# Kernel optimization log

Hardware: AMD Instinct MI355X
Metric: run time of the kernel (lower is better)

## Reference

```python
import jax, jax.numpy as jnp
import numpy as np

C = 0.01          # ToPoincare curvature hardcoded in get_dist
K = 5             # k_way (s0..s4 hardcoded in source)
N = 5             # n_shot
Q = 15            # queries per class -> LQ = K*Q = 75
D = 1024          # feature dim (hardcoded reshape(1,-1,1024))
TEMP = 1.0
N_AUG = 40
MIN_NORM = 1e-5


def _artanh(x):
    return jnp.arctanh(jnp.clip(x, -1 + 1e-5, 1 - 1e-5))


def _project(x, c):
    norm = jnp.maximum(jnp.linalg.norm(x, axis=-1, keepdims=True), MIN_NORM)
    maxnorm = (1 - 1e-3) / jnp.sqrt(c)
    return jnp.where(norm > maxnorm, x / norm * maxnorm, x)


def _expmap0(u, c):
    sc = jnp.sqrt(c)
    un = jnp.maximum(jnp.linalg.norm(u, axis=-1, keepdims=True), MIN_NORM)
    return jnp.tanh(sc * un) * u / (sc * un)


def _mobius_add(x, y, c):
    x2 = jnp.sum(x * x, -1, keepdims=True)
    y2 = jnp.sum(y * y, -1, keepdims=True)
    xy = jnp.sum(x * y, -1, keepdims=True)
    num = (1 + 2 * c * xy + c * y2) * x + (1 - c * x2) * y
    den = 1 + 2 * c * xy + c * c * x2 * y2
    return num / jnp.maximum(den, MIN_NORM)


def _expmap(x, u, c):
    # exp map at point x of tangent vector u
    sc = jnp.sqrt(c)
    un = jnp.maximum(jnp.linalg.norm(u, axis=-1, keepdims=True), MIN_NORM)
    lam = 2.0 / jnp.maximum(1 - c * jnp.sum(x * x, -1, keepdims=True), MIN_NORM)
    second = jnp.tanh(sc * lam * un / 2) * u / (sc * un)
    return _mobius_add(x, second, c)


def _ptransp0_p(x, v, c):
    # parallel transport of v from the origin to x
    return v * (1 - c * jnp.sum(x * x, -1, keepdims=True))


def _dist_matrix(x, y, c):
    # pairwise Poincare distance [n, m] without materializing [n,m,d]:
    # ||(-x) (+) y||^2 = a^2 x2 + b^2 y2 - 2ab<x,y>, a = 1-2c<x,y>+c y2, b = 1-c x2
    sc = jnp.sqrt(c)
    x2 = jnp.sum(x * x, -1)[:, None]
    y2 = jnp.sum(y * y, -1)[None, :]
    xy = x @ y.T
    a = 1 - 2 * c * xy + c * y2
    b = 1 - c * x2
    num2 = a * a * x2 + b * b * y2 - 2 * a * b * xy
    den = 1 - 2 * c * xy + c * c * x2 * y2
    norm = jnp.sqrt(jnp.maximum(num2, 0.0)) / jnp.maximum(den, MIN_NORM)
    return 2.0 / sc * _artanh(sc * norm)


def _p2k(x, c):
    return 2 * x / (1 + c * jnp.sum(x * x, -1, keepdims=True))


def _k2p(x, c):
    return x / (1 + jnp.sqrt(jnp.maximum(1 - c * jnp.sum(x * x, -1, keepdims=True), 0.0)))


def _poincare_mean_masked(x, mask, c):
    # Einstein-midpoint Poincare mean over rows of x weighted by {0,1} mask
    k = _p2k(x, c)
    lam = 1.0 / jnp.sqrt(jnp.maximum(1 - c * jnp.sum(k * k, -1), MIN_NORM))
    w = lam * mask
    mean_k = (w[:, None] * k).sum(0) / w.sum()
    return _k2p(mean_k, c)


def setup_inputs() -> dict:
    key = jax.random.key(0)
    k1, k2, k3 = jax.random.split(key, 3)
    feat = jax.random.normal(k1, (K * N + K * Q, D), dtype=jnp.float32)
    label = jax.random.randint(k2, (2, K * Q), 0, K)
    noise = jax.random.normal(k3, (K, N_AUG, D), dtype=jnp.float32)
    return {"feat": feat, "label": label, "noise": noise}


def reference(feat, label, noise):
    support_e = feat[: N * K].reshape(K, N, D)
    queries_e = feat[N * K:]                                  # [LQ, D]
    support_p_ = _project(_expmap0(feat[: N * K], C), C).reshape(K, N, D)
    queries_p = _project(_expmap0(queries_e, C), C)           # [LQ, D]

    ones_n = jnp.ones((N,), feat.dtype)
    proto_p = jax.vmap(lambda s: _poincare_mean_masked(s, ones_n, C))(support_p_)  # [K, D]
    dist = _dist_matrix(queries_p, proto_p, C) / TEMP          # [LQ, K]
    pred = jnp.argmax(-dist, 1)                                # [LQ]
    qmask = (pred[:, None] == jnp.arange(K)[None, :]).astype(feat.dtype)  # [LQ, K]

    def per_class(sup_p, sup_e, mq, nz):
        # sup_p/sup_e: [N,D]; mq: [LQ] routing mask; nz: [N_AUG,D] unit normals
        m = jnp.concatenate([ones_n, mq])                      # [N+LQ]
        pts_p = jnp.concatenate([sup_p, queries_p], 0)
        pts_e = jnp.concatenate([sup_e, queries_e], 0)
        s_p = _poincare_mean_masked(pts_p, m, C)               # [D] augmented proto
        cnt = m.sum()
        mu = (m[:, None] * pts_e).sum(0) / cnt
        var = (m[:, None] * (pts_e - mu) ** 2).sum(0) / (cnt - 1)  # unbiased, as torch.std
        std = jnp.sqrt(var)                                    # [D]
        v = nz * std                                           # torch.normal(0, std), 40 samples
        pt = _ptransp0_p(s_p[None, :], v, C)
        ex = _expmap(s_p[None, :], pt, C)                      # [N_AUG, D]
        s_new = jnp.concatenate([sup_p, ex], 0)                # [N+N_AUG, D]
        return _poincare_mean_masked(s_new, jnp.ones((N + N_AUG,), feat.dtype), C)

    proto_new = jax.vmap(per_class, in_axes=(0, 0, 1, 0))(support_p_, support_e, qmask, noise)
    dist_new = _dist_matrix(queries_p, proto_new, C) / TEMP

    y_pred = jax.nn.softmax(-dist_new, axis=1)
    log_p_y = jax.nn.log_softmax(-dist, axis=1)
    # nn.CrossEntropyLoss applied to log-probs (double log-softmax, faithful to source)
    ll = jax.nn.log_softmax(log_p_y, axis=1)
    lbl = label[1]
    loss = -jnp.mean(jnp.take_along_axis(ll, lbl[:, None], axis=1))
    return y_pred, loss
```

## Files before the change

### kernel.cpp

```cpp
#include <hip/hip_runtime.h>
#include <hip/hip_bf16.h>
#include <math.h>

#define CCd     0.01
#define SCd     0.1
#define MAXNRMd 9.99
#define MINNd   1e-5
#define DD      1024
#define NK      25
#define NQ      75
#define NROWS   100
#define KCLS    5
#define NAUG    40

__device__ __forceinline__ double wave_reduce_d(double v){
#pragma unroll
  for (int o = 32; o > 0; o >>= 1) v += __shfl_xor(v, o);
  return v;
}

__device__ __forceinline__ double hyp_dist_d(double xy, double x2, double y2){
  double a    = 1.0 - 2.0*CCd*xy + CCd*y2;
  double b    = 1.0 - CCd*x2;
  double num2 = a*a*x2 + b*b*y2 - 2.0*a*b*xy;
  double den  = 1.0 - 2.0*CCd*xy + CCd*CCd*x2*y2;
  double nrm  = sqrt(fmax(num2, 0.0)) / fmax(den, MINNd);
  double z    = SCd * nrm;
  z = fmin(fmax(z, -1.0 + MINNd), 1.0 - MINNd);
  return 10.0 * log((1.0 + z) / (1.0 - z));
}

__global__ __launch_bounds__(256)
void k_expmap(const float* __restrict__ feat, float* __restrict__ P,
              double* __restrict__ p2d){
  const int r = blockIdx.x, t = threadIdx.x;
  const float4 v = reinterpret_cast<const float4*>(feat + r*DD)[t];
  double ss = (double)v.x*v.x + (double)v.y*v.y + (double)v.z*v.z + (double)v.w*v.w;
  __shared__ double red[4];
  ss = wave_reduce_d(ss);
  if ((t & 63) == 0) red[t >> 6] = ss;
  __syncthreads();
  ss = red[0] + red[1] + red[2] + red[3];
  double un = fmax(sqrt(ss), MINNd);
  double th = tanh(SCd*un);
  double na = th * 10.0;
  double factor, pn;
  if (na > MAXNRMd) { factor = MAXNRMd/un; pn = MAXNRMd; }
  else              { factor = th/(SCd*un); pn = na; }
  float4 o;
  o.x = (float)(v.x*factor); o.y = (float)(v.y*factor);
  o.z = (float)(v.z*factor); o.w = (float)(v.w*factor);
  reinterpret_cast<float4*>(P + r*DD)[t] = o;
  if (t == 0) p2d[r] = pn*pn;
}

__global__ __launch_bounds__(1024)
void k_proto(const float* __restrict__ P, const double* __restrict__ p2d,
             float* __restrict__ protoP, double* __restrict__ proto2d){
  const int c = blockIdx.x, t = threadIdx.x;
  double la[5], wsum = 0.0;
#pragma unroll
  for (int i = 0; i < 5; i++){
    double pp = p2d[c*5+i];
    double a  = 2.0/(1.0 + CCd*pp);
    double k2 = a*a*pp;
    double l  = 1.0/sqrt(fmax(1.0 - CCd*k2, MINNd));
    la[i] = l*a; wsum += l;
  }
  double s = 0.0;
#pragma unroll
  for (int i = 0; i < 5; i++) s += la[i]*(double)P[(c*5+i)*DD + t];
  s /= wsum;
  __shared__ double red[16];
  double ss = wave_reduce_d(s*s);
  if ((t & 63) == 0) red[t >> 6] = ss;
  __syncthreads();
  ss = 0.0;
#pragma unroll
  for (int i = 0; i < 16; i++) ss += red[i];
  double sf = 1.0/(1.0 + sqrt(fmax(1.0 - CCd*ss, 0.0)));
  protoP[c*DD + t] = (float)(s*sf);
  if (t == 0) proto2d[c] = ss*sf*sf;
}

__global__ __launch_bounds__(256)
void k_dist1(const float* __restrict__ P, const float* __restrict__ protoP,
             const double* __restrict__ p2d, const double* __restrict__ proto2d,
             double* __restrict__ distS, int* __restrict__ predS){
  const int q = blockIdx.x, t = threadIdx.x;
  const float* xq = P + (NK+q)*DD;
  double acc[5] = {0,0,0,0,0};
#pragma unroll
  for (int k = 0; k < 4; k++){
    int d = t + 256*k;
    double x = (double)xq[d];
#pragma unroll
    for (int c = 0; c < 5; c++) acc[c] += x*(double)protoP[c*DD + d];
  }
  __shared__ double red[4][5];
#pragma unroll
  for (int c = 0; c < 5; c++) acc[c] = wave_reduce_d(acc[c]);
  if ((t & 63) == 0){
#pragma unroll
    for (int c = 0; c < 5; c++) red[t >> 6][c] = acc[c];
  }
  __syncthreads();
  if (t == 0){
    double x2 = p2d[NK+q];
    double best = 1e300; int bi = 0;
#pragma unroll
    for (int c = 0; c < 5; c++){
      double dot = red[0][c] + red[1][c] + red[2][c] + red[3][c];
      double dv  = hyp_dist_d(dot, x2, proto2d[c]);
      distS[q*5 + c] = dv;
      if (dv < best){ best = dv; bi = c; }
    }
    predS[q] = bi;
  }
}

__global__ __launch_bounds__(1024)
void k_aug(const float* __restrict__ feat, const float* __restrict__ noise,
           const float* __restrict__ P, const double* __restrict__ p2d,
           const int* __restrict__ predS,
           float* __restrict__ protoN, double* __restrict__ protoN2d){
  const int c = blockIdx.x, t = threadIdx.x;
  const int wave = t >> 6, lane = t & 63;
  __shared__ double wA[80], wL[80], wM[80];
  __shared__ int    rows[80];
  __shared__ double scal[8];
  __shared__ double spS[DD], stdS[DD];
  __shared__ double coefSj[NAUG], coefVj[NAUG], lamJ[NAUG];
  __shared__ double red[16];

  if (t < 80){
    int row; double m;
    if (t < 5){ row = c*5 + t; m = 1.0; }
    else      { row = NK + (t-5); m = (predS[t-5] == c) ? 1.0 : 0.0; }
    rows[t] = row;
    double pp = p2d[row];
    double a  = 2.0/(1.0 + CCd*pp);
    double k2 = a*a*pp;
    double l  = 1.0/sqrt(fmax(1.0 - CCd*k2, MINNd));
    wA[t] = m*l*a; wL[t] = m*l; wM[t] = m;
  }
  __syncthreads();
  if (t == 0){
    double wsum = 0.0, cnt = 0.0;
    for (int i = 0; i < 80; i++){ wsum += wL[i]; cnt += wM[i]; }
    scal[0] = wsum; scal[1] = cnt;
  }
  __syncthreads();
  const double wsum = scal[0], cnt = scal[1];

  {
    const int d = t;
    double mkd = 0.0, mud = 0.0, sqd = 0.0;
    for (int i = 0; i < 80; i++){
      int row = rows[i];
      mkd += wA[i]*(double)P[row*DD + d];
      double e = (double)feat[row*DD + d];
      mud += wM[i]*e;
      sqd += wM[i]*e*e;
    }
    mkd /= wsum;
    mud /= cnt;
    double var = (sqd - cnt*mud*mud)/(cnt - 1.0);
    stdS[d] = sqrt(fmax(var, 0.0));
    double s = wave_reduce_d(mkd*mkd);
    if (lane == 0) red[wave] = s;
    __syncthreads();
    double mk2 = 0.0;
#pragma unroll
    for (int i = 0; i < 16; i++) mk2 += red[i];
    double sf = 1.0/(1.0 + sqrt(fmax(1.0 - CCd*mk2, 0.0)));
    spS[d] = mkd*sf;
    if (t == 0) scal[2] = mk2*sf*sf;
  }
  __syncthreads();
  const double sp2  = scal[2];
  const double lamx = 2.0/fmax(1.0 - CCd*sp2, MINNd);
  const double ptf  = 1.0 - CCd*sp2;

  for (int j = wave; j < NAUG; j += 16){
    const float* nzr = noise + (c*NAUG + j)*DD;
    double s_un2 = 0.0, s_dot = 0.0;
#pragma unroll
    for (int k = 0; k < 16; k++){
      int d = lane + 64*k;
      double v = (double)nzr[d]*stdS[d];
      s_un2 += v*v;
      s_dot += v*spS[d];
    }
#pragma unroll
    for (int o = 32; o > 0; o >>= 1){
      s_un2 += __shfl_xor(s_un2, o);
      s_dot += __shfl_xor(s_dot, o);
    }
    if (lane == 0){
      double unv = sqrt(s_un2);
      double unp = fmax(ptf*unv, MINNd);
      double g0  = tanh(SCd*lamx*unp*0.5)/(SCd*unp);
      double g   = g0*ptf;
      double y2  = g*g*s_un2;
      double xy  = g*s_dot;
      double A   = 1.0 + 2.0*CCd*xy + CCd*y2;
      double B   = ptf;
      double den = fmax(1.0 + 2.0*CCd*xy + CCd*CCd*sp2*y2, MINNd);
      double ex2 = (A*A*sp2 + 2.0*A*B*g*s_dot + B*B*g*g*s_un2)/(den*den);
      double ae  = 2.0/(1.0 + CCd*ex2);
      double k2e = ae*ae*ex2;
      double le  = 1.0/sqrt(fmax(1.0 - CCd*k2e, MINNd));
      coefSj[j] = le*ae*A/den;
      coefVj[j] = le*ae*B*g/den;
      lamJ[j]   = le;
    }
  }
  __syncthreads();
  if (t == 0){
    double lsum = 0.0, sS = 0.0;
#pragma unroll
    for (int i = 0; i < 5; i++){
      double pp = p2d[c*5+i];
      double a  = 2.0/(1.0 + CCd*pp);
      double k2 = a*a*pp;
      double l  = 1.0/sqrt(fmax(1.0 - CCd*k2, MINNd));
      lsum += l;
    }
    for (int j = 0; j < NAUG; j++){ lsum += lamJ[j]; sS += coefSj[j]; }
    scal[3] = lsum; scal[4] = sS;
  }
  __syncthreads();
  const double lamsum = scal[3], sumS = scal[4];

  {
    const int d = t;
    double val = sumS*spS[d];
#pragma unroll
    for (int i = 0; i < 5; i++) val += wA[i]*(double)P[(c*5+i)*DD + d];
    double nacc = 0.0;
    for (int j = 0; j < NAUG; j++) nacc += coefVj[j]*(double)noise[(c*NAUG + j)*DD + d];
    val += stdS[d]*nacc;
    val /= lamsum;
    double s = wave_reduce_d(val*val);
    if (lane == 0) red[wave] = s;
    __syncthreads();
    double mk2 = 0.0;
#pragma unroll
    for (int i = 0; i < 16; i++) mk2 += red[i];
    double sf = 1.0/(1.0 + sqrt(fmax(1.0 - CCd*mk2, 0.0)));
    protoN[c*DD + d] = (float)(val*sf);
    if (t == 0) protoN2d[c] = mk2*sf*sf;
  }
}

__global__ __launch_bounds__(256)
void k_dist2(const float* __restrict__ P, const float* __restrict__ protoN,
             const double* __restrict__ p2d, const double* __restrict__ protoN2d,
             const double* __restrict__ distS, const int* __restrict__ label,
             float* __restrict__ out, double* __restrict__ lossQ){
  const int q = blockIdx.x, t = threadIdx.x;
  const float* xq = P + (NK+q)*DD;
  double acc[5] = {0,0,0,0,0};
#pragma unroll
  for (int k = 0; k < 4; k++){
    int d = t + 256*k;
    double x = (double)xq[d];
#pragma unroll
    for (int c = 0; c < 5; c++) acc[c] += x*(double)protoN[c*DD + d];
  }
  __shared__ double red[4][5];
#pragma unroll
  for (int c = 0; c < 5; c++) acc[c] = wave_reduce_d(acc[c]);
  if ((t & 63) == 0){
#pragma unroll
    for (int c = 0; c < 5; c++) red[t >> 6][c] = acc[c];
  }
  __syncthreads();
  if (t == 0){
    double x2 = p2d[NK+q];
    double v[5]; double mx = -1e300;
#pragma unroll
    for (int c = 0; c < 5; c++){
      double dot = red[0][c] + red[1][c] + red[2][c] + red[3][c];
      v[c] = -hyp_dist_d(dot, x2, protoN2d[c]);
      mx = fmax(mx, v[c]);
    }
    double se = 0.0;
#pragma unroll
    for (int c = 0; c < 5; c++){ v[c] = exp(v[c]-mx); se += v[c]; }
    double inv = 1.0/se;
#pragma unroll
    for (int c = 0; c < 5; c++) out[q*5 + c] = (float)(v[c]*inv);

    double u[5]; mx = -1e300;
#pragma unroll
    for (int c = 0; c < 5; c++){ u[c] = -distS[q*5+c]; mx = fmax(mx, u[c]); }
    double s1 = 0.0;
#pragma unroll
    for (int c = 0; c < 5; c++) s1 += exp(u[c]-mx);
    double lse1 = mx + log(s1);
#pragma unroll
    for (int c = 0; c < 5; c++) u[c] -= lse1;
    double mx2 = -1e300;
#pragma unroll
    for (int c = 0; c < 5; c++) mx2 = fmax(mx2, u[c]);
    double s2 = 0.0;
#pragma unroll
    for (int c = 0; c < 5; c++) s2 += exp(u[c]-mx2);
    double lse2 = mx2 + log(s2);
    lossQ[q] = u[label[NQ + q]] - lse2;
  }
}

__global__ __launch_bounds__(128)
void k_loss(const double* __restrict__ lossQ, float* __restrict__ out){
  const int t = threadIdx.x;
  double v = (t < NQ) ? lossQ[t] : 0.0;
  v = wave_reduce_d(v);
  __shared__ double red[2];
  if ((t & 63) == 0) red[t >> 6] = v;
  __syncthreads();
  if (t == 0) out[NQ*KCLS] = (float)(-(red[0]+red[1])/75.0);
}

extern "C" void kernel_launch(void* const* d_in, const int* in_sizes, int n_in,
                              void* d_out, int out_size, void* d_ws, size_t ws_size,
                              hipStream_t stream) {
  const float* feat  = (const float*)d_in[0];
  const int*   label = (const int*)d_in[1];
  const float* noise = (const float*)d_in[2];
  float* out = (float*)d_out;

  float*  P        = (float*)d_ws;
  float*  protoP   = P + NROWS*DD;
  float*  protoN   = protoP + KCLS*DD;
  double* p2d      = (double*)(protoN + KCLS*DD);
  double* proto2d  = p2d + NROWS;
  double* protoN2d = proto2d + KCLS;
  double* distS    = protoN2d + KCLS;
  double* lossQ    = distS + NQ*KCLS;
  int*    predS    = (int*)(lossQ + NQ);

  k_expmap<<<NROWS, 256, 0, stream>>>(feat, P, p2d);
  k_proto <<<KCLS, 1024, 0, stream>>>(P, p2d, protoP, proto2d);
  k_dist1 <<<NQ, 256, 0, stream>>>(P, protoP, p2d, proto2d, distS, predS);
  k_aug   <<<KCLS, 1024, 0, stream>>>(feat, noise, P, p2d, predS, protoN, protoN2d);
  k_dist2 <<<NQ, 256, 0, stream>>>(P, protoN, p2d, protoN2d, distS, label, out, lossQ);
  k_loss  <<<1, 128, 0, stream>>>(lossQ, out);
}
```

Measured before the change: 119.9 us.

## Split per-class augmentation kernel into stats, coef, assembly kernels across more blocks

The single 5-block k_aug kernel (1024 threads each) is replaced by three kernels: k_stats (20 blocks over feature chunks), k_coef (200 blocks, one per augmented sample) and k_asm (20 blocks). Normalisation scales are deferred, so partial squared norms are passed between kernels and the Klein-to-Poincare factor is applied later, including inside k_dist2. This spreads a serial, low-occupancy stage across many more CUs. It costs two extra launches and global round-trips for the intermediate std and mean vectors.

New measurement: 98.29 us. 18.0% less time.

```diff
diff --git a/kernel.cpp b/kernel.cpp
--- a/kernel.cpp
+++ b/kernel.cpp
@@ -28,6 +28,13 @@
   double z    = SCd * nrm;
   z = fmin(fmax(z, -1.0 + MINNd), 1.0 - MINNd);
   return 10.0 * log((1.0 + z) / (1.0 - z));
+}
+
+__device__ __forceinline__ void kweights(double pp, double* la, double* l_out){
+  double a  = 2.0/(1.0 + CCd*pp);
+  double k2 = a*a*pp;
+  double l  = 1.0/sqrt(fmax(1.0 - CCd*k2, MINNd));
+  *la = l*a; *l_out = l;
 }
 
 __global__ __launch_bounds__(256)
@@ -61,11 +68,9 @@
   double la[5], wsum = 0.0;
 #pragma unroll
   for (int i = 0; i < 5; i++){
-    double pp = p2d[c*5+i];
-    double a  = 2.0/(1.0 + CCd*pp);
-    double k2 = a*a*pp;
-    double l  = 1.0/sqrt(fmax(1.0 - CCd*k2, MINNd));
-    la[i] = l*a; wsum += l;
+    double lam;
+    kweights(p2d[c*5+i], &la[i], &lam);
+    wsum += lam;
   }
   double s = 0.0;
 #pragma unroll
@@ -119,30 +124,21 @@
   }
 }
 
-__global__ __launch_bounds__(1024)
-void k_aug(const float* __restrict__ feat, const float* __restrict__ noise,
-           const float* __restrict__ P, const double* __restrict__ p2d,
-           const int* __restrict__ predS,
-           float* __restrict__ protoN, double* __restrict__ protoN2d){
-  const int c = blockIdx.x, t = threadIdx.x;
-  const int wave = t >> 6, lane = t & 63;
-  __shared__ double wA[80], wL[80], wM[80];
-  __shared__ int    rows[80];
-  __shared__ double scal[8];
-  __shared__ double spS[DD], stdS[DD];
-  __shared__ double coefSj[NAUG], coefVj[NAUG], lamJ[NAUG];
-  __shared__ double red[16];
-
+__global__ __launch_bounds__(256)
+void k_stats(const float* __restrict__ feat, const float* __restrict__ P,
+             const double* __restrict__ p2d, const int* __restrict__ predS,
+             double* __restrict__ std_g, double* __restrict__ mkr_g,
+             double* __restrict__ mk2part){
+  const int c = blockIdx.x >> 2, chunk = blockIdx.x & 3, t = threadIdx.x;
+  __shared__ double wA[80], wL[80], wM[80], scal[2], red[4];
+  __shared__ int rows[80];
   if (t < 80){
     int row; double m;
     if (t < 5){ row = c*5 + t; m = 1.0; }
     else      { row = NK + (t-5); m = (predS[t-5] == c) ? 1.0 : 0.0; }
     rows[t] = row;
-    double pp = p2d[row];
-    double a  = 2.0/(1.0 + CCd*pp);
-    double k2 = a*a*pp;
-    double l  = 1.0/sqrt(fmax(1.0 - CCd*k2, MINNd));
-    wA[t] = m*l*a; wL[t] = m*l; wM[t] = m;
+    double la, l; kweights(p2d[row], &la, &l);
+    wA[t] = m*la; wL[t] = m*l; wM[t] = m;
   }
   __syncthreads();
   if (t == 0){
@@ -152,111 +148,117 @@
   }
   __syncthreads();
   const double wsum = scal[0], cnt = scal[1];
-
-  {
-    const int d = t;
-    double mkd = 0.0, mud = 0.0, sqd = 0.0;
-    for (int i = 0; i < 80; i++){
-      int row = rows[i];
-      mkd += wA[i]*(double)P[row*DD + d];
-      double e = (double)feat[row*DD + d];
-      mud += wM[i]*e;
-      sqd += wM[i]*e*e;
+  const int d = chunk*256 + t;
+  double mkd = 0.0, mud = 0.0, sqd = 0.0;
+  for (int i = 0; i < 80; i++){
+    int row = rows[i];
+    mkd += wA[i]*(double)P[row*DD + d];
+    double e = (double)feat[row*DD + d];
+    mud += wM[i]*e;
+    sqd += wM[i]*e*e;
+  }
+  mkd /= wsum;
+  mud /= cnt;
+  double var = (sqd - cnt*mud*mud)/(cnt - 1.0);
+  std_g[c*DD + d] = sqrt(fmax(var, 0.0));
+  mkr_g[c*DD + d] = mkd;
+  double s = wave_reduce_d(mkd*mkd);
+  if ((t & 63) == 0) red[t >> 6] = s;
+  __syncthreads();
+  if (t == 0) mk2part[blockIdx.x] = red[0] + red[1] + red[2] + red[3];
+}
+
+__global__ __launch_bounds__(256)
+void k_coef(const float* __restrict__ noise, const double* __restrict__ std_g,
+            const double* __restrict__ mkr_g, const double* __restrict__ mk2part,
+            double* __restrict__ coefS_g, double* __restrict__ coefV_g,
+            double* __restrict__ lamJ_g){
+  const int j = blockIdx.x, c = blockIdx.y, t = threadIdx.x;
+  const float*  nzr = noise + (c*NAUG + j)*DD;
+  const double* st  = std_g + c*DD;
+  const double* mk  = mkr_g + c*DD;
+  double un2 = 0.0, rd = 0.0;
+#pragma unroll
+  for (int k = 0; k < 4; k++){
+    int d = t + 256*k;
+    double v = (double)nzr[d]*st[d];
+    un2 += v*v;
+    rd  += v*mk[d];
+  }
+  __shared__ double red[4][2];
+  un2 = wave_reduce_d(un2);
+  rd  = wave_reduce_d(rd);
+  if ((t & 63) == 0){ red[t >> 6][0] = un2; red[t >> 6][1] = rd; }
+  __syncthreads();
+  if (t == 0){
+    double s_un2 = red[0][0]+red[1][0]+red[2][0]+red[3][0];
+    double rdot  = red[0][1]+red[1][1]+red[2][1]+red[3][1];
+    double mk2 = mk2part[c*4+0]+mk2part[c*4+1]+mk2part[c*4+2]+mk2part[c*4+3];
+    double sf  = 1.0/(1.0 + sqrt(fmax(1.0 - CCd*mk2, 0.0)));
+    double sp2 = mk2*sf*sf;
+    double lamx = 2.0/fmax(1.0 - CCd*sp2, MINNd);
+    double ptf  = 1.0 - CCd*sp2;
+    double s_dot = sf*rdot;
+    double unv = sqrt(s_un2);
+    double unp = fmax(ptf*unv, MINNd);
+    double g0  = tanh(SCd*lamx*unp*0.5)/(SCd*unp);
+    double g   = g0*ptf;
+    double y2  = g*g*s_un2;
+    double xy  = g*s_dot;
+    double A   = 1.0 + 2.0*CCd*xy + CCd*y2;
+    double B   = ptf;
+    double den = fmax(1.0 + 2.0*CCd*xy + CCd*CCd*sp2*y2, MINNd);
+    double ex2 = (A*A*sp2 + 2.0*A*B*g*s_dot + B*B*g*g*s_un2)/(den*den);
+    double ae  = 2.0/(1.0 + CCd*ex2);
+    double k2e = ae*ae*ex2;
+    double le  = 1.0/sqrt(fmax(1.0 - CCd*k2e, MINNd));
+    coefS_g[c*NAUG + j] = le*ae*A/den;
+    coefV_g[c*NAUG + j] = le*ae*B*g/den;
+    lamJ_g[c*NAUG + j]  = le;
+  }
+}
+
+__global__ __launch_bounds__(256)
+void k_asm(const float* __restrict__ noise, const float* __restrict__ P,
+           const double* __restrict__ p2d, const double* __restrict__ std_g,
+           const double* __restrict__ mkr_g, const double* __restrict__ mk2part,
+           const double* __restrict__ coefS_g, const double* __restrict__ coefV_g,
+           const double* __restrict__ lamJ_g,
+           float* __restrict__ protoNr, double* __restrict__ mk2Np){
+  const int c = blockIdx.x >> 2, chunk = blockIdx.x & 3, t = threadIdx.x;
+  __shared__ double cV[NAUG], supC[5], scal[3], red[4];
+  if (t < NAUG) cV[t] = coefV_g[c*NAUG + t];
+  if (t == 0){
+    double lsum = 0.0, sS = 0.0;
+#pragma unroll
+    for (int i = 0; i < 5; i++){
+      double la, l; kweights(p2d[c*5+i], &la, &l);
+      supC[i] = la; lsum += l;
     }
-    mkd /= wsum;
-    mud /= cnt;
-    double var = (sqd - cnt*mud*mud)/(cnt - 1.0);
-    stdS[d] = sqrt(fmax(var, 0.0));
-    double s = wave_reduce_d(mkd*mkd);
-    if (lane == 0) red[wave] = s;
-    __syncthreads();
-    double mk2 = 0.0;
-#pragma unroll
-    for (int i = 0; i < 16; i++) mk2 += red[i];
-    double sf = 1.0/(1.0 + sqrt(fmax(1.0 - CCd*mk2, 0.0)));
-    spS[d] = mkd*sf;
-    if (t == 0) scal[2] = mk2*sf*sf;
-  }
-  __syncthreads();
-  const double sp2  = scal[2];
-  const double lamx = 2.0/fmax(1.0 - CCd*sp2, MINNd);
-  const double ptf  = 1.0 - CCd*sp2;
-
-  for (int j = wave; j < NAUG; j += 16){
-    const float* nzr = noise + (c*NAUG + j)*DD;
-    double s_un2 = 0.0, s_dot = 0.0;
-#pragma unroll
-    for (int k = 0; k < 16; k++){
-      int d = lane + 64*k;
-      double v = (double)nzr[d]*stdS[d];
-      s_un2 += v*v;
-      s_dot += v*spS[d];
-    }
-#pragma unroll
-    for (int o = 32; o > 0; o >>= 1){
-      s_un2 += __shfl_xor(s_un2, o);
-      s_dot += __shfl_xor(s_dot, o);
-    }
-    if (lane == 0){
-      double unv = sqrt(s_un2);
-      double unp = fmax(ptf*unv, MINNd);
-      double g0  = tanh(SCd*lamx*unp*0.5)/(SCd*unp);
-      double g   = g0*ptf;
-      double y2  = g*g*s_un2;
-      double xy  = g*s_dot;
-      double A   = 1.0 + 2.0*CCd*xy + CCd*y2;
-      double B   = ptf;
-      double den = fmax(1.0 + 2.0*CCd*xy + CCd*CCd*sp2*y2, MINNd);
-      double ex2 = (A*A*sp2 + 2.0*A*B*g*s_dot + B*B*g*g*s_un2)/(den*den);
-      double ae  = 2.0/(1.0 + CCd*ex2);
-      double k2e = ae*ae*ex2;
-      double le  = 1.0/sqrt(fmax(1.0 - CCd*k2e, MINNd));
-      coefSj[j] = le*ae*A/den;
-      coefVj[j] = le*ae*B*g/den;
-      lamJ[j]   = le;
-    }
-  }
-  __syncthreads();
-  if (t == 0){
-    double lsum = 0.0, sS = 0.0;
-#pragma unroll
-    for (int i = 0; i < 5; i++){
-      double pp = p2d[c*5+i];
-      double a  = 2.0/(1.0 + CCd*pp);
-      double k2 = a*a*pp;
-      double l  = 1.0/sqrt(fmax(1.0 - CCd*k2, MINNd));
-      lsum += l;
-    }
-    for (int j = 0; j < NAUG; j++){ lsum += lamJ[j]; sS += coefSj[j]; }
-    scal[3] = lsum; scal[4] = sS;
-  }
-  __syncthreads();
-  const double lamsum = scal[3], sumS = scal[4];
-
-  {
-    const int d = t;
-    double val = sumS*spS[d];
-#pragma unroll
-    for (int i = 0; i < 5; i++) val += wA[i]*(double)P[(c*5+i)*DD + d];
-    double nacc = 0.0;
-    for (int j = 0; j < NAUG; j++) nacc += coefVj[j]*(double)noise[(c*NAUG + j)*DD + d];
-    val += stdS[d]*nacc;
-    val /= lamsum;
-    double s = wave_reduce_d(val*val);
-    if (lane == 0) red[wave] = s;
-    __syncthreads();
-    double mk2 = 0.0;
-#pragma unroll
-    for (int i = 0; i < 16; i++) mk2 += red[i];
-    double sf = 1.0/(1.0 + sqrt(fmax(1.0 - CCd*mk2, 0.0)));
-    protoN[c*DD + d] = (float)(val*sf);
-    if (t == 0) protoN2d[c] = mk2*sf*sf;
-  }
-}
-
-__global__ __launch_bounds__(256)
-void k_dist2(const float* __restrict__ P, const float* __restrict__ protoN,
-             const double* __restrict__ p2d, const double* __restrict__ protoN2d,
+    for (int j = 0; j < NAUG; j++){ lsum += lamJ_g[c*NAUG+j]; sS += coefS_g[c*NAUG+j]; }
+    double mk2 = mk2part[c*4+0]+mk2part[c*4+1]+mk2part[c*4+2]+mk2part[c*4+3];
+    double sf  = 1.0/(1.0 + sqrt(fmax(1.0 - CCd*mk2, 0.0)));
+    scal[0] = lsum; scal[1] = sS; scal[2] = sf;
+  }
+  __syncthreads();
+  const int d = chunk*256 + t;
+  double val = scal[1]*scal[2]*mkr_g[c*DD + d];
+#pragma unroll
+  for (int i = 0; i < 5; i++) val += supC[i]*(double)P[(c*5+i)*DD + d];
+  double na = 0.0;
+  for (int j = 0; j < NAUG; j++) na += cV[j]*(double)noise[(c*NAUG + j)*DD + d];
+  val += std_g[c*DD + d]*na;
+  val /= scal[0];
+  protoNr[c*DD + d] = (float)val;
+  double s = wave_reduce_d(val*val);
+  if ((t & 63) == 0) red[t >> 6] = s;
+  __syncthreads();
+  if (t == 0) mk2Np[blockIdx.x] = red[0] + red[1] + red[2] + red[3];
+}
+
+__global__ __launch_bounds__(256)
+void k_dist2(const float* __restrict__ P, const float* __restrict__ protoNr,
+             const double* __restrict__ p2d, const double* __restrict__ mk2Np,
              const double* __restrict__ distS, const int* __restrict__ label,
              float* __restrict__ out, double* __restrict__ lossQ){
   const int q = blockIdx.x, t = threadIdx.x;
@@ -267,7 +269,7 @@
     int d = t + 256*k;
     double x = (double)xq[d];
 #pragma unroll
-    for (int c = 0; c < 5; c++) acc[c] += x*(double)protoN[c*DD + d];
+    for (int c = 0; c < 5; c++) acc[c] += x*(double)protoNr[c*DD + d];
   }
   __shared__ double red[4][5];
 #pragma unroll
@@ -282,8 +284,11 @@
     double v[5]; double mx = -1e300;
 #pragma unroll
     for (int c = 0; c < 5; c++){
-      double dot = red[0][c] + red[1][c] + red[2][c] + red[3][c];
-      v[c] = -hyp_dist_d(dot, x2, protoN2d[c]);
+      double mk2N = mk2Np[c*4+0]+mk2Np[c*4+1]+mk2Np[c*4+2]+mk2Np[c*4+3];
+      double sfN  = 1.0/(1.0 + sqrt(fmax(1.0 - CCd*mk2N, 0.0)));
+      double dot  = sfN*(red[0][c] + red[1][c] + red[2][c] + red[3][c]);
+      double y2   = mk2N*sfN*sfN;
+      v[c] = -hyp_dist_d(dot, x2, y2);
       mx = fmax(mx, v[c]);
     }
     double se = 0.0;
@@ -334,18 +339,28 @@
 
   float*  P        = (float*)d_ws;
   float*  protoP   = P + NROWS*DD;
-  float*  protoN   = protoP + KCLS*DD;
-  double* p2d      = (double*)(protoN + KCLS*DD);
+  float*  protoNr  = protoP + KCLS*DD;
+  double* p2d      = (double*)(protoNr + KCLS*DD);
   double* proto2d  = p2d + NROWS;
-  double* protoN2d = proto2d + KCLS;
-  double* distS    = protoN2d + KCLS;
+  double* distS    = proto2d + KCLS;
   double* lossQ    = distS + NQ*KCLS;
-  int*    predS    = (int*)(lossQ + NQ);
+  double* std_g    = lossQ + NQ;
+  double* mkr_g    = std_g + KCLS*DD;
+  double* mk2part  = mkr_g + KCLS*DD;
+  double* coefS_g  = mk2part + 4*KCLS;
+  double* coefV_g  = coefS_g + KCLS*NAUG;
+  double* lamJ_g   = coefV_g + KCLS*NAUG;
+  double* mk2Np    = lamJ_g + KCLS*NAUG;
+  int*    predS    = (int*)(mk2Np + 4*KCLS);
 
   k_expmap<<<NROWS, 256, 0, stream>>>(feat, P, p2d);
   k_proto <<<KCLS, 1024, 0, stream>>>(P, p2d, protoP, proto2d);
   k_dist1 <<<NQ, 256, 0, stream>>>(P, protoP, p2d, proto2d, distS, predS);
-  k_aug   <<<KCLS, 1024, 0, stream>>>(feat, noise, P, p2d, predS, protoN, protoN2d);
-  k_dist2 <<<NQ, 256, 0, stream>>>(P, protoN, p2d, protoN2d, distS, label, out, lossQ);
+  k_stats <<<4*KCLS, 256, 0, stream>>>(feat, P, p2d, predS, std_g, mkr_g, mk2part);
+  k_coef  <<<dim3(NAUG, KCLS), 256, 0, stream>>>(noise, std_g, mkr_g, mk2part,
+                                                 coefS_g, coefV_g, lamJ_g);
+  k_asm   <<<4*KCLS, 256, 0, stream>>>(noise, P, p2d, std_g, mkr_g, mk2part,
+                                       coefS_g, coefV_g, lamJ_g, protoNr, mk2Np);
+  k_dist2 <<<NQ, 256, 0, stream>>>(P, protoNr, p2d, mk2Np, distS, label, out, lossQ);
   k_loss  <<<1, 128, 0, stream>>>(lossQ, out);
 }
```
